# Kernel optimization log

Measured on AMD Instinct MI355X. Metric: run time of the kernel, lower is better.

The kernel has to match this reference:

```python
import jax, jax.numpy as jnp
import numpy as np

# --- problem constants (match init_kwargs / input_specs) ---
FS = 50.0            # sampling rate (Hz)
WINDOW_FREQ = 0.5    # running-abs-mean window (Hz); >0 -> RAM whitening branch
F1, F2 = 0.1, 10.0   # taper corner frequencies (Hz)
NCH, NPTS = 1000, 30000
XCOR = 2 * NPTS - 1          # 59999
FAST = 65536                 # nextpow2(XCOR)


def setup_inputs() -> dict:
    key = jax.random.key(0)
    k1, k2 = jax.random.split(key)
    return {
        "data1": jax.random.normal(k1, (NCH, NPTS), dtype=jnp.float32),
        "data2": jax.random.normal(k2, (NCH, NPTS), dtype=jnp.float32),
    }


def _running_abs_mean_whiten(rfft, nwin):
    """Vectorized equivalent of per-channel running_absolute_mean:
    pad |spec| by nwin edge values each side, box-filter (scipy 'same'
    alignment => window tmp[i+off+1 : i+off+1+nwin], off=(nwin-1)//2),
    then divide spectrum by the smoothed magnitude."""
    nch, nf = rfft.shape
    off = (nwin - 1) // 2
    a = jnp.abs(rfft)  # [nch, nf]
    tmp = jnp.concatenate(
        [jnp.broadcast_to(a[:, :1], (nch, nwin)), a,
         jnp.broadcast_to(a[:, -1:], (nch, nwin))], axis=1)  # [nch, nf+2*nwin]
    cs = jnp.pad(jnp.cumsum(tmp, axis=1), ((0, 0), (1, 0)))   # leading zero
    smoothed = (cs[:, off + 1 + nwin: off + 1 + nwin + nf]
                - cs[:, off + 1: off + 1 + nf]) / nwin
    return jnp.nan_to_num(rfft / smoothed)


def _spectral_whitening(rfft, df):
    nf = rfft.shape[-1]
    idxf1 = int(np.floor(F1 / df))
    idxf2 = int(np.ceil(F2 / df))
    nwin = int(WINDOW_FREQ / df)
    w = _running_abs_mean_whiten(rfft, nwin)
    # cosine-squared tapers outside [f1, f2]
    taper_lo = jnp.cos(jnp.linspace(np.pi / 2, np.pi, idxf1)) ** 2
    taper_hi = jnp.cos(jnp.linspace(np.pi, np.pi / 2, nf - idxf2)) ** 2
    w = w.at[:, :idxf1].multiply(taper_lo)
    w = w.at[:, idxf2:].multiply(taper_hi)
    return w


def reference(data1, data2):
    df = FS / FAST
    f1 = jnp.fft.rfft(data1, n=FAST, axis=-1)
    f2 = jnp.fft.rfft(data2, n=FAST, axis=-1)
    f1 = _spectral_whitening(f1, df)
    f2 = _spectral_whitening(f2, df)
    cc = jnp.fft.irfft(jnp.conj(f1) * f2, n=FAST, axis=-1)  # [nch, FAST]
    cc = jnp.roll(cc, FAST // 2, axis=-1)
    start = FAST // 2 - XCOR // 2
    return cc[:, start:start + XCOR]  # [nch, 2*npts-1]
```

## Files before the change

kernel.cpp:

```cpp
#include <hip/hip_runtime.h>

#define PI_F 3.14159265358979323846f

#define NCH   1000
#define NPTS  30000
#define NHALF 15000
#define NFFT  32768
#define NBF32 1024
#define STR   32770
#define XCOR  59999

#define UC 0.99518472667219693f
#define US 0.09801714032956060f

__device__ __forceinline__ float2 cadd(float2 a, float2 b){ return make_float2(a.x+b.x, a.y+b.y); }
__device__ __forceinline__ float2 csub(float2 a, float2 b){ return make_float2(a.x-b.x, a.y-b.y); }
__device__ __forceinline__ float2 cmul(float2 a, float2 b){ return make_float2(a.x*b.x - a.y*b.y, a.x*b.y + a.y*b.x); }
__device__ __forceinline__ float2 conjmul(float2 a, float2 b){
  return make_float2(a.x*b.x + a.y*b.y, a.x*b.y - a.y*b.x);
}

template<int S>
__device__ __forceinline__ float2 mulIs(float2 z){ return make_float2(-(float)S*z.y, (float)S*z.x); }

template<int S>
__device__ __forceinline__ void dft8(float2 v[8]){
  const float r2 = 0.7071067811865476f;
  const float sf = (float)S;
  float2 ea=cadd(v[0],v[4]), eb=csub(v[0],v[4]);
  float2 ec=cadd(v[2],v[6]), ed=csub(v[2],v[6]);
  float2 oa=cadd(v[1],v[5]), ob=csub(v[1],v[5]);
  float2 oc=cadd(v[3],v[7]), od=csub(v[3],v[7]);
  float2 ied=mulIs<S>(ed), iod=mulIs<S>(od);
  float2 E0=cadd(ea,ec), E2=csub(ea,ec), E1=cadd(eb,ied), E3=csub(eb,ied);
  float2 O0=cadd(oa,oc), O2=csub(oa,oc), O1=cadd(ob,iod), O3=csub(ob,iod);
  float2 T1 = make_float2(r2*(O1.x - sf*O1.y), r2*(O1.y + sf*O1.x));
  float2 T2 = mulIs<S>(O2);
  float2 T3 = make_float2(r2*(-O3.x - sf*O3.y), r2*(sf*O3.x - O3.y));
  v[0]=cadd(E0,O0); v[4]=csub(E0,O0);
  v[1]=cadd(E1,T1); v[5]=csub(E1,T1);
  v[2]=cadd(E2,T2); v[6]=csub(E2,T2);
  v[3]=cadd(E3,T3); v[7]=csub(E3,T3);
}

template<int S>
__device__ __forceinline__ void dft4(float2 v[4]){
  float2 t0=cadd(v[0],v[2]), t1=csub(v[0],v[2]);
  float2 t2=cadd(v[1],v[3]), t3=mulIs<S>(csub(v[1],v[3]));
  v[0]=cadd(t0,t2); v[2]=csub(t0,t2);
  v[1]=cadd(t1,t3); v[3]=csub(t1,t3);
}

template<int S>
__device__ __forceinline__ void dft32(float2 v[32]){
  constexpr float TC[22] = {
    1.f, 0.98078528040323044f, 0.92387953251128674f, 0.83146961230254524f,
    0.70710678118654757f, 0.55557023301960218f, 0.38268343236508978f, 0.19509032201612825f,
    0.f, -0.19509032201612825f, -0.38268343236508978f, -0.55557023301960218f,
    -0.70710678118654757f, -0.83146961230254524f, -0.92387953251128674f, -0.98078528040323044f,
    -1.f, -0.98078528040323044f, -0.92387953251128674f, -0.83146961230254524f,
    -0.70710678118654757f, -0.55557023301960218f };
  constexpr float TS[22] = {
    0.f, 0.19509032201612825f, 0.38268343236508978f, 0.55557023301960218f,
    0.70710678118654757f, 0.83146961230254524f, 0.92387953251128674f, 0.98078528040323044f,
    1.f, 0.98078528040323044f, 0.92387953251128674f, 0.83146961230254524f,
    0.70710678118654757f, 0.55557023301960218f, 0.38268343236508978f, 0.19509032201612825f,
    0.f, -0.19509032201612825f, -0.38268343236508978f, -0.55557023301960218f,
    -0.70710678118654757f, -0.83146961230254524f };
  float2 y[4][8];
  #pragma unroll
  for (int b = 0; b < 4; ++b)
    #pragma unroll
    for (int a = 0; a < 8; ++a) y[b][a] = v[4*a + b];
  #pragma unroll
  for (int b = 0; b < 4; ++b) dft8<S>(y[b]);
  #pragma unroll
  for (int b = 1; b < 4; ++b)
    #pragma unroll
    for (int k1 = 1; k1 < 8; ++k1) {
      int m = b*k1;
      float2 w = make_float2(TC[m], (float)S * TS[m]);
      y[b][k1] = cmul(y[b][k1], w);
    }
  #pragma unroll
  for (int k1 = 0; k1 < 8; ++k1) {
    float2 z[4] = { y[0][k1], y[1][k1], y[2][k1], y[3][k1] };
    dft4<S>(z);
    #pragma unroll
    for (int k2 = 0; k2 < 4; ++k2) v[k1 + 8*k2] = z[k2];
  }
}

template<int S>
__device__ __forceinline__ void stage_twiddle32(float2 v[32], float ang){
  float s1,c1,s8,c8;
  __sincosf(ang, &s1, &c1);
  __sincosf(8.f*ang, &s8, &c8);
  float2 w1 = make_float2(c1, s1), w8 = make_float2(c8, s8);
  float2 w16 = cmul(w8, w8), w24 = cmul(w16, w8);
  float2 base[4] = { make_float2(1.f, 0.f), w8, w16, w24 };
  #pragma unroll
  for (int m = 0; m < 4; ++m) {
    float2 wr = base[m];
    if (m > 0) v[8*m] = cmul(v[8*m], wr);
    #pragma unroll
    for (int l = 1; l < 8; ++l) { wr = cmul(wr, w1); v[8*m+l] = cmul(v[8*m+l], wr); }
  }
}

__global__ __launch_bounds__(256) void fft_fwd_fused(const float* __restrict__ d1, const float* __restrict__ d2,
                                                     float2* __restrict__ out, int cb, int ch0)
{
  __shared__ float2 lds[256*33];
  const int bid = blockIdx.x;
  const int c = bid >> 2, b = bid & 3;
  const int t = threadIdx.x;
  const float* src = (c < cb) ? (d1 + (size_t)(ch0 + c) * NPTS)
                              : (d2 + (size_t)(ch0 + c - cb) * NPTS);
  const float2* src2 = reinterpret_cast<const float2*>(src);

  const int j1 = 8*b + (t & 7) + 32*(t >> 3);
  float2 v[32];
  #pragma unroll
  for (int r = 0; r < 32; ++r) {
    int m = j1 + (r << 10);
    v[r] = (m < NHALF) ? src2[m] : make_float2(0.f, 0.f);
  }
  dft32<-1>(v);
  #pragma unroll
  for (int r = 0; r < 32; ++r) lds[t*33 + r] = v[r];
  __syncthreads();

  const int d = t >> 5, jm = t & 31;
  #pragma unroll
  for (int r = 0; r < 32; ++r) v[r] = lds[(d + 8*r)*33 + jm];
  stage_twiddle32<-1>(v, -(2.0f*PI_F) * (float)jm * (1.0f/1024.0f));
  dft32<-1>(v);
  const int j2 = 256*b + t;
  float2* dst = out + (size_t)c * STR + ((j2 >> 5) << 10) + jm;
  #pragma unroll
  for (int r = 0; r < 32; ++r) dst[(size_t)(r << 5)] = v[r];
}

template<int LG, int S>
__global__ __launch_bounds__(256) void fft_pass32(const float2* __restrict__ in, float2* __restrict__ out)
{
  int tid = blockIdx.x*256 + threadIdx.x;
  int c = tid >> 10;
  int j = tid & (NBF32-1);
  const float2* src = in + (size_t)c * STR;
  float2 v[32];
  #pragma unroll
  for (int r = 0; r < 32; ++r) v[r] = src[j + (r << 10)];
  constexpr int NS = 1 << LG;
  int jm = j & (NS - 1);
  if constexpr (LG > 0) {
    float ang = (float)S * (2.0f*PI_F) * (float)jm / (float)(NS*32);
    stage_twiddle32<S>(v, ang);
  }
  dft32<S>(v);
  int idxD = ((j >> LG) << (LG+5)) + jm;
  float2* dst = out + (size_t)c * STR + idxD;
  #pragma unroll
  for (int r = 0; r < 32; ++r) dst[(size_t)(r << LG)] = v[r];
}

__device__ __forceinline__ int padidx(int m){ return m + (m >> 5); }

__global__ __launch_bounds__(1024) void whiten_kernel(float2* __restrict__ buf)
{
  const int ch = blockIdx.x;
  const int t  = threadIdx.x;
  float2* Z = buf + (size_t)ch * STR;
  __shared__ float s[33793];
  __shared__ float wsums[16];

  float2 X[33];
  {
    float s0, c0; __sincosf(-PI_F*(float)t*(1.0f/32768.0f), &s0, &c0);
    float2 uw = make_float2(c0, s0);
    const float2 uwstep = make_float2(UC, -US);
    #pragma unroll
    for (int i = 0; i < 33; ++i) {
      int k = i*1024 + t;
      if (i < 32 || t == 0) {
        float2 zk = Z[k & (NFFT-1)];
        float2 zn = Z[(NFFT - k) & (NFFT-1)];
        float2 xe = make_float2(0.5f*(zk.x+zn.x), 0.5f*(zk.y-zn.y));
        float2 xh = make_float2(0.5f*(zk.x-zn.x), 0.5f*(zk.y+zn.y));
        float2 xo = make_float2(xh.y, -xh.x);
        X[i] = cadd(xe, cmul(uw, xo));
        s[padidx(k)] = sqrtf(X[i].x*X[i].x + X[i].y*X[i].y);
      }
      uw = cmul(uw, uwstep);
    }
  }
  __syncthreads();

  const int base = t*32;
  float sum = 0.f;
  #pragma unroll
  for (int q = 0; q < 32; ++q) sum += s[padidx(base+q)];
  if (t == 1023) sum += s[padidx(32768)];
  const int lane = t & 63, wid = t >> 6;
  float v = sum;
  #pragma unroll
  for (int off = 1; off < 64; off <<= 1) {
    float u = __shfl_up(v, off);
    if (lane >= off) v += u;
  }
  if (lane == 63) wsums[wid] = v;
  __syncthreads();
  float wexcl = 0.f;
  for (int w = 0; w < 16; ++w) wexcl += (w < wid) ? wsums[w] : 0.f;
  float run = wexcl + (v - sum);
  #pragma unroll
  for (int q = 0; q < 32; ++q) {
    int idx = padidx(base+q);
    run += s[idx];
    s[idx] = run;
  }
  if (t == 1023) { int idx = padidx(32768); run += s[idx]; s[idx] = run; }
  __syncthreads();

  const float a0 = s[padidx(0)];
  const float alast = s[padidx(32768)] - s[padidx(32767)];
  {
    float su, cu; __sincosf(((float)t - 13108.0f)*(PI_F/39320.0f), &su, &cu);
    float2 tu = make_float2(cu, su);
    float tss, tcc; __sincosf(1024.0f*(PI_F/39320.0f), &tss, &tcc);
    const float2 tustep = make_float2(tcc, tss);
    #pragma unroll
    for (int i = 0; i < 33; ++i) {
      int k = i*1024 + t;
      if (i < 32 || t == 0) {
        int hi = k + 327; if (hi > 32768) hi = 32768;
        int lom1 = k - 328;
        float Shi = s[padidx(hi)];
        float Slo = (lom1 >= 0) ? s[padidx(lom1)] : 0.f;
        float lc = (k < 327) ? (float)(327 - k) : 0.f;
        float rc = (k > 32441) ? (float)(k - 32441) : 0.f;
        float smoothed = (lc*a0 + (Shi - Slo) + rc*alast) * (1.0f/655.0f);
        float2 wv;
        if (smoothed > 0.f) {
          float inv = 1.0f / smoothed;
          wv = make_float2(X[i].x*inv, X[i].y*inv);
        } else wv = make_float2(0.f, 0.f);
        float tp = 1.0f;
        if (k < 131)        { float sn = __sinf((float)k * (PI_F/260.0f)); tp = sn*sn; }
        else if (k >= 13108) tp = tu.x*tu.x;
        wv.x *= tp; wv.y *= tp;
        Z[k] = wv;
      }
      tu = cmul(tu, tustep);
    }
  }
}

__device__ __forceinline__ float2 pack_zinv(float2 Ck, float2 Cm, float2 pw){
  const float scale = 1.0f/32768.0f;
  float2 xe = make_float2(0.5f*(Ck.x+Cm.x), 0.5f*(Ck.y-Cm.y));
  float2 d  = make_float2(0.5f*(Ck.x-Cm.x), 0.5f*(Ck.y+Cm.y));
  float2 xo = cmul(pw, d);
  return make_float2((xe.x - xo.y)*scale, (xe.y + xo.x)*scale);
}

__global__ __launch_bounds__(256) void cross_inv0_pair(const float2* __restrict__ W,
                                                       float2* __restrict__ out0, int cb)
{
  __shared__ float2 zbs[256*33];
  const int bid = blockIdx.x;
  const int c = bid >> 1;
  const int t = threadIdx.x;
  const int p = ((bid & 1) << 8) + t;
  const float2* W1 = W + (size_t)c * STR;
  const float2* W2 = W + (size_t)(cb + c) * STR;
  const float scale = 1.0f/32768.0f;
  float2 zA[32];
  float2* zB = zbs + t*33;

  if (p != 0) {
    const int q = 1024 - p;
    float sp, cp; __sincosf(PI_F*(float)p*(1.0f/32768.0f), &sp, &cp);
    float2 pw = make_float2(cp, sp);
    const float2 pstep = make_float2(UC, US);
    #pragma unroll
    for (int r = 0; r < 32; ++r) {
      int m  = p + (r << 10);
      int mm = q + ((31 - r) << 10);
      float2 Ck = conjmul(W1[m],  W2[m]);
      float2 Cm = conjmul(W1[mm], W2[mm]);
      zA[r]    = pack_zinv(Ck, Cm, pw);
      zB[31-r] = pack_zinv(Cm, Ck, make_float2(-pw.x, pw.y));
      pw = cmul(pw, pstep);
    }
  } else {
    {
      float2 Ck = conjmul(W1[0], W2[0]);
      float2 Cm = conjmul(W1[32768], W2[32768]);
      zA[0] = pack_zinv(Ck, Cm, make_float2(1.f, 0.f));
    }
    #pragma unroll
    for (int i = 1; i < 16; ++i) {
      int k = i << 10, km = 32768 - k;
      float2 Ck = conjmul(W1[k],  W2[k]);
      float2 Cm = conjmul(W1[km], W2[km]);
      float sp2, cp2; __sincosf(PI_F*(float)k*(1.0f/32768.0f), &sp2, &cp2);
      zA[i]    = pack_zinv(Ck, Cm, make_float2(cp2, sp2));
      zA[32-i] = pack_zinv(Cm, Ck, make_float2(-cp2, sp2));
    }
    {
      float2 Ck = conjmul(W1[16384], W2[16384]);
      zA[16] = make_float2(Ck.x*scale, -Ck.y*scale);
    }
    #pragma unroll
    for (int i = 0; i < 16; ++i) {
      int k = (i << 10) + 512, km = 32768 - k;
      float2 Ck = conjmul(W1[k],  W2[k]);
      float2 Cm = conjmul(W1[km], W2[km]);
      float sp2, cp2; __sincosf(PI_F*(float)k*(1.0f/32768.0f), &sp2, &cp2);
      zB[i]    = pack_zinv(Ck, Cm, make_float2(cp2, sp2));
      zB[31-i] = pack_zinv(Cm, Ck, make_float2(-cp2, sp2));
    }
  }

  dft32<1>(zA);
  {
    float4* o4 = reinterpret_cast<float4*>(out0 + (size_t)c*STR + (size_t)p*32);
    #pragma unroll
    for (int r = 0; r < 32; r += 2)
      o4[r>>1] = make_float4(zA[r].x, zA[r].y, zA[r+1].x, zA[r+1].y);
  }
  {
    float2 zq[32];
    #pragma unroll
    for (int r = 0; r < 32; ++r) zq[r] = zB[r];
    dft32<1>(zq);
    const int jout = (p == 0) ? 512 : (1024 - p);
    float4* o4 = reinterpret_cast<float4*>(out0 + (size_t)c*STR + (size_t)jout*32);
    #pragma unroll
    for (int r = 0; r < 32; r += 2)
      o4[r>>1] = make_float4(zq[r].x, zq[r].y, zq[r+1].x, zq[r+1].y);
  }
}

__global__ __launch_bounds__(256) void fft_inv_final32(const float2* __restrict__ in, float* __restrict__ out, int ch0)
{
  int tid = blockIdx.x*256 + threadIdx.x;
  int c = tid >> 10;
  int j = tid & (NBF32-1);
  const float2* src = in + (size_t)c * STR;
  float2 v[32];
  #pragma unroll
  for (int r = 0; r < 32; ++r) v[r] = src[j + (r << 10)];
  float ang = (2.0f*PI_F) * (float)j * (1.0f/32768.0f);
  stage_twiddle32<1>(v, ang);
  dft32<1>(v);
  float* o = out + (size_t)(ch0 + c) * XCOR;
  #pragma unroll
  for (int r = 0; r < 32; ++r) {
    int n = j + (r << 10);
    int m = 2*n;
    int j1 = (m <= 29999) ? (m + 29999) : ((m >= 35537) ? (m - 35537) : -1);
    if (j1 >= 0) o[j1] = v[r].x;
    int m2 = m + 1;
    int j2 = (m2 <= 29999) ? (m2 + 29999) : ((m2 >= 35537) ? (m2 - 35537) : -1);
    if (j2 >= 0) o[j2] = v[r].y;
  }
}

__global__ void diag_kernel(float* out, float vv){ if (threadIdx.x==0 && blockIdx.x==0) out[0] = vv; }

extern "C" void kernel_launch(void* const* d_in, const int* in_sizes, int n_in,
                              void* d_out, int out_size, void* d_ws, size_t ws_size,
                              hipStream_t stream)
{
  const float* d1 = (const float*)d_in[0];
  const float* d2 = (const float*)d_in[1];
  float* out = (float*)d_out;

  const size_t bytesPerCh = 2ULL * 2ULL * (size_t)STR * sizeof(float2);
  int CB = (int)(ws_size / bytesPerCh);
  if (CB > NCH) CB = NCH;
  if (CB < 1) { diag_kernel<<<1,1,0,stream>>>(out, (float)ws_size); return; }

  float2* bufA = (float2*)d_ws;
  float2* bufB = bufA + (size_t)2 * CB * STR;

  for (int ch0 = 0; ch0 < NCH; ch0 += CB) {
    int cb = (NCH - ch0 < CB) ? (NCH - ch0) : CB;
    int nch2 = 2*cb;
    dim3 thr(256);

    fft_fwd_fused     <<<dim3(nch2*4), thr, 0, stream>>>(d1, d2, bufA, cb, ch0);
    fft_pass32<10,-1> <<<dim3(nch2*4), thr, 0, stream>>>(bufA, bufB);

    whiten_kernel     <<<dim3(nch2), dim3(1024), 0, stream>>>(bufB);

    cross_inv0_pair   <<<dim3(cb*2), thr, 0, stream>>>(bufB, bufA, cb);

    fft_pass32<5,1>   <<<dim3(cb*4), thr, 0, stream>>>(bufA, bufB);
    fft_inv_final32   <<<dim3(cb*4), thr, 0, stream>>>(bufB, out, ch0);
  }
}
```

Measured before the change: 1.180 ms.

## Store real whitening gain and apply it inside the cross-spectrum kernel

The whitening kernel no longer holds the unpacked spectrum in 33 registers per thread or writes a whitened complex spectrum back. It writes only a real per-bin gain, taper divided by the smoothed magnitude. The cross-spectrum kernel then re-derives the spectrum from the packed FFT output, applies the gains and forms the conjugate product. This is meant to cut register pressure in the 1024-thread whitening kernel and halve its write traffic. In exchange the cross kernel does extra unpack arithmetic and reads an additional gain array.

```diff
diff --git a/kernel.cpp b/kernel.cpp
--- a/kernel.cpp
+++ b/kernel.cpp
@@ -8,6 +8,7 @@
 #define NFFT  32768
 #define NBF32 1024
 #define STR   32770
+#define GSTR  32770
 #define XCOR  59999
 
 #define UC 0.99518472667219693f
@@ -167,15 +168,16 @@
 
 __device__ __forceinline__ int padidx(int m){ return m + (m >> 5); }
 
-__global__ __launch_bounds__(1024) void whiten_kernel(float2* __restrict__ buf)
+__global__ __launch_bounds__(1024) void whiten_scan(const float2* __restrict__ zbuf,
+                                                    float* __restrict__ gbase)
 {
   const int ch = blockIdx.x;
   const int t  = threadIdx.x;
-  float2* Z = buf + (size_t)ch * STR;
+  const float2* Z = zbuf + (size_t)ch * STR;
+  float* G = gbase + (size_t)ch * GSTR;
   __shared__ float s[33793];
   __shared__ float wsums[16];
 
-  float2 X[33];
   {
     float s0, c0; __sincosf(-PI_F*(float)t*(1.0f/32768.0f), &s0, &c0);
     float2 uw = make_float2(c0, s0);
@@ -189,8 +191,8 @@
         float2 xe = make_float2(0.5f*(zk.x+zn.x), 0.5f*(zk.y-zn.y));
         float2 xh = make_float2(0.5f*(zk.x-zn.x), 0.5f*(zk.y+zn.y));
         float2 xo = make_float2(xh.y, -xh.x);
-        X[i] = cadd(xe, cmul(uw, xo));
-        s[padidx(k)] = sqrtf(X[i].x*X[i].x + X[i].y*X[i].y);
+        float2 Xi = cadd(xe, cmul(uw, xo));
+        s[padidx(k)] = sqrtf(Xi.x*Xi.x + Xi.y*Xi.y);
       }
       uw = cmul(uw, uwstep);
     }
@@ -241,16 +243,10 @@
         float lc = (k < 327) ? (float)(327 - k) : 0.f;
         float rc = (k > 32441) ? (float)(k - 32441) : 0.f;
         float smoothed = (lc*a0 + (Shi - Slo) + rc*alast) * (1.0f/655.0f);
-        float2 wv;
-        if (smoothed > 0.f) {
-          float inv = 1.0f / smoothed;
-          wv = make_float2(X[i].x*inv, X[i].y*inv);
-        } else wv = make_float2(0.f, 0.f);
         float tp = 1.0f;
         if (k < 131)        { float sn = __sinf((float)k * (PI_F/260.0f)); tp = sn*sn; }
         else if (k >= 13108) tp = tu.x*tu.x;
-        wv.x *= tp; wv.y *= tp;
-        Z[k] = wv;
+        G[k] = (smoothed > 0.f) ? tp / smoothed : 0.f;
       }
       tu = cmul(tu, tustep);
     }
@@ -265,62 +261,111 @@
   return make_float2((xe.x - xo.y)*scale, (xe.y + xo.x)*scale);
 }
 
-__global__ __launch_bounds__(256) void cross_inv0_pair(const float2* __restrict__ W,
-                                                       float2* __restrict__ out0, int cb)
+__device__ __forceinline__ void unpack_w(float2 zk, float2 zm, float2 u, float2& Xn, float2& Xm){
+  float2 xe = make_float2(0.5f*(zk.x+zm.x), 0.5f*(zk.y-zm.y));
+  float2 xh = make_float2(0.5f*(zk.x-zm.x), 0.5f*(zk.y+zm.y));
+  float2 xo = make_float2(xh.y, -xh.x);
+  float2 pr = cmul(u, xo);
+  Xn = make_float2(xe.x+pr.x, xe.y+pr.y);
+  Xm = make_float2(xe.x-pr.x, -(xe.y-pr.y));
+}
+
+__global__ __launch_bounds__(256) void cross_inv0_pair_v2(const float2* __restrict__ Zb,
+                                                          const float* __restrict__ gbase,
+                                                          float2* __restrict__ out0, int cb)
 {
   __shared__ float2 zbs[256*33];
   const int bid = blockIdx.x;
   const int c = bid >> 1;
   const int t = threadIdx.x;
   const int p = ((bid & 1) << 8) + t;
-  const float2* W1 = W + (size_t)c * STR;
-  const float2* W2 = W + (size_t)(cb + c) * STR;
+  const float2* Z1 = Zb + (size_t)c * STR;
+  const float2* Z2 = Zb + (size_t)(cb + c) * STR;
+  const float* G1 = gbase + (size_t)c * GSTR;
+  const float* G2 = gbase + (size_t)(cb + c) * GSTR;
   const float scale = 1.0f/32768.0f;
   float2 zA[32];
   float2* zB = zbs + t*33;
 
   if (p != 0) {
-    const int q = 1024 - p;
-    float sp, cp; __sincosf(PI_F*(float)p*(1.0f/32768.0f), &sp, &cp);
-    float2 pw = make_float2(cp, sp);
-    const float2 pstep = make_float2(UC, US);
+    float su, cu; __sincosf(-PI_F*(float)p*(1.0f/32768.0f), &su, &cu);
+    float2 u = make_float2(cu, su);
+    const float2 ustep = make_float2(UC, -US);
     #pragma unroll
     for (int r = 0; r < 32; ++r) {
       int m  = p + (r << 10);
-      int mm = q + ((31 - r) << 10);
-      float2 Ck = conjmul(W1[m],  W2[m]);
-      float2 Cm = conjmul(W1[mm], W2[mm]);
+      int mm = 32768 - m;
+      float2 X1n, X1m, X2n, X2m;
+      unpack_w(Z1[m], Z1[mm], u, X1n, X1m);
+      unpack_w(Z2[m], Z2[mm], u, X2n, X2m);
+      float g1m = G1[m], g1mm = G1[mm], g2m = G2[m], g2mm = G2[mm];
+      float2 W1m  = make_float2(X1n.x*g1m,  X1n.y*g1m);
+      float2 W1mm = make_float2(X1m.x*g1mm, X1m.y*g1mm);
+      float2 W2m  = make_float2(X2n.x*g2m,  X2n.y*g2m);
+      float2 W2mm = make_float2(X2m.x*g2mm, X2m.y*g2mm);
+      float2 Ck = conjmul(W1m,  W2m);
+      float2 Cm = conjmul(W1mm, W2mm);
+      float2 pw = make_float2(u.x, -u.y);
       zA[r]    = pack_zinv(Ck, Cm, pw);
       zB[31-r] = pack_zinv(Cm, Ck, make_float2(-pw.x, pw.y));
-      pw = cmul(pw, pstep);
+      u = cmul(u, ustep);
     }
   } else {
     {
-      float2 Ck = conjmul(W1[0], W2[0]);
-      float2 Cm = conjmul(W1[32768], W2[32768]);
+      float2 z0 = Z1[0], y0 = Z2[0];
+      float2 X1n = make_float2(z0.x + z0.y, 0.f), X1m = make_float2(z0.x - z0.y, 0.f);
+      float2 X2n = make_float2(y0.x + y0.y, 0.f), X2m = make_float2(y0.x - y0.y, 0.f);
+      float2 W10 = make_float2(X1n.x*G1[0], 0.f),     W20 = make_float2(X2n.x*G2[0], 0.f);
+      float2 W1N = make_float2(X1m.x*G1[32768], 0.f), W2N = make_float2(X2m.x*G2[32768], 0.f);
+      float2 Ck = conjmul(W10, W20);
+      float2 Cm = conjmul(W1N, W2N);
       zA[0] = pack_zinv(Ck, Cm, make_float2(1.f, 0.f));
     }
     #pragma unroll
     for (int i = 1; i < 16; ++i) {
-      int k = i << 10, km = 32768 - k;
-      float2 Ck = conjmul(W1[k],  W2[k]);
-      float2 Cm = conjmul(W1[km], W2[km]);
-      float sp2, cp2; __sincosf(PI_F*(float)k*(1.0f/32768.0f), &sp2, &cp2);
-      zA[i]    = pack_zinv(Ck, Cm, make_float2(cp2, sp2));
-      zA[32-i] = pack_zinv(Cm, Ck, make_float2(-cp2, sp2));
+      int m = i << 10, mm = 32768 - m;
+      float su, cu; __sincosf(-PI_F*(float)m*(1.0f/32768.0f), &su, &cu);
+      float2 u = make_float2(cu, su);
+      float2 X1n, X1m, X2n, X2m;
+      unpack_w(Z1[m], Z1[mm], u, X1n, X1m);
+      unpack_w(Z2[m], Z2[mm], u, X2n, X2m);
+      float g1m = G1[m], g1mm = G1[mm], g2m = G2[m], g2mm = G2[mm];
+      float2 W1m  = make_float2(X1n.x*g1m,  X1n.y*g1m);
+      float2 W1mm = make_float2(X1m.x*g1mm, X1m.y*g1mm);
+      float2 W2m  = make_float2(X2n.x*g2m,  X2n.y*g2m);
+      float2 W2mm = make_float2(X2m.x*g2mm, X2m.y*g2mm);
+      float2 Ck = conjmul(W1m,  W2m);
+      float2 Cm = conjmul(W1mm, W2mm);
+      float2 pw = make_float2(u.x, -u.y);
+      zA[i]    = pack_zinv(Ck, Cm, pw);
+      zA[32-i] = pack_zinv(Cm, Ck, make_float2(-pw.x, pw.y));
     }
     {
-      float2 Ck = conjmul(W1[16384], W2[16384]);
-      zA[16] = make_float2(Ck.x*scale, -Ck.y*scale);
+      float2 z16 = Z1[16384], y16 = Z2[16384];
+      float2 X1 = make_float2(z16.x, -z16.y), X2 = make_float2(y16.x, -y16.y);
+      float g1 = G1[16384], g2 = G2[16384];
+      float2 W1 = make_float2(X1.x*g1, X1.y*g1), W2 = make_float2(X2.x*g2, X2.y*g2);
+      float2 C16 = conjmul(W1, W2);
+      zA[16] = make_float2(C16.x*scale, -C16.y*scale);
     }
     #pragma unroll
     for (int i = 0; i < 16; ++i) {
-      int k = (i << 10) + 512, km = 32768 - k;
-      float2 Ck = conjmul(W1[k],  W2[k]);
-      float2 Cm = conjmul(W1[km], W2[km]);
-      float sp2, cp2; __sincosf(PI_F*(float)k*(1.0f/32768.0f), &sp2, &cp2);
-      zB[i]    = pack_zinv(Ck, Cm, make_float2(cp2, sp2));
-      zB[31-i] = pack_zinv(Cm, Ck, make_float2(-cp2, sp2));
+      int m = (i << 10) + 512, mm = 32768 - m;
+      float su, cu; __sincosf(-PI_F*(float)m*(1.0f/32768.0f), &su, &cu);
+      float2 u = make_float2(cu, su);
+      float2 X1n, X1m, X2n, X2m;
+      unpack_w(Z1[m], Z1[mm], u, X1n, X1m);
+      unpack_w(Z2[m], Z2[mm], u, X2n, X2m);
+      float g1m = G1[m], g1mm = G1[mm], g2m = G2[m], g2mm = G2[mm];
+      float2 W1m  = make_float2(X1n.x*g1m,  X1n.y*g1m);
+      float2 W1mm = make_float2(X1m.x*g1mm, X1m.y*g1mm);
+      float2 W2m  = make_float2(X2n.x*g2m,  X2n.y*g2m);
+      float2 W2mm = make_float2(X2m.x*g2mm, X2m.y*g2mm);
+      float2 Ck = conjmul(W1m,  W2m);
+      float2 Cm = conjmul(W1mm, W2mm);
+      float2 pw = make_float2(u.x, -u.y);
+      zB[i]    = pack_zinv(Ck, Cm, pw);
+      zB[31-i] = pack_zinv(Cm, Ck, make_float2(-pw.x, pw.y));
     }
   }
 
@@ -386,20 +431,22 @@
 
   float2* bufA = (float2*)d_ws;
   float2* bufB = bufA + (size_t)2 * CB * STR;
+  float*  gbase = (float*)bufA;
+  float2* out0  = bufA + (size_t)CB * STR;
 
   for (int ch0 = 0; ch0 < NCH; ch0 += CB) {
     int cb = (NCH - ch0 < CB) ? (NCH - ch0) : CB;
     int nch2 = 2*cb;
     dim3 thr(256);
 
-    fft_fwd_fused     <<<dim3(nch2*4), thr, 0, stream>>>(d1, d2, bufA, cb, ch0);
-    fft_pass32<10,-1> <<<dim3(nch2*4), thr, 0, stream>>>(bufA, bufB);
-
-    whiten_kernel     <<<dim3(nch2), dim3(1024), 0, stream>>>(bufB);
-
-    cross_inv0_pair   <<<dim3(cb*2), thr, 0, stream>>>(bufB, bufA, cb);
-
-    fft_pass32<5,1>   <<<dim3(cb*4), thr, 0, stream>>>(bufA, bufB);
-    fft_inv_final32   <<<dim3(cb*4), thr, 0, stream>>>(bufB, out, ch0);
-  }
-}
+    fft_fwd_fused      <<<dim3(nch2*4), thr, 0, stream>>>(d1, d2, bufA, cb, ch0);
+    fft_pass32<10,-1>  <<<dim3(nch2*4), thr, 0, stream>>>(bufA, bufB);
+
+    whiten_scan        <<<dim3(nch2), dim3(1024), 0, stream>>>(bufB, gbase);
+
+    cross_inv0_pair_v2 <<<dim3(cb*2), thr, 0, stream>>>(bufB, gbase, out0, cb);
+
+    fft_pass32<5,1>    <<<dim3(cb*4), thr, 0, stream>>>(out0, bufB);
+    fft_inv_final32    <<<dim3(cb*4), thr, 0, stream>>>(bufB, out, ch0);
+  }
+}
```

Result: slower. 1.312 ms (+11.2%).
